# Performance work log

Measured on AMD Instinct MI355X. Metric: run time of the kernel, lower is better.

The kernel has to match this reference:

```python
import jax, jax.numpy as jnp
import numpy as np

B, D = 8192, 128


def setup_inputs() -> dict:
    key = jax.random.key(0)
    ks = jax.random.split(key, 7)
    s = 1.0 / np.sqrt(D)  # torch Linear default init scale
    x = jax.random.normal(ks[0], (B, D), jnp.float32)
    W1 = jax.random.uniform(ks[1], (D, D), jnp.float32, -s, s)
    b1 = jax.random.uniform(ks[2], (D,), jnp.float32, -s, s)
    Wmu = jax.random.uniform(ks[3], (D, D), jnp.float32, -s, s)
    bmu = jax.random.uniform(ks[4], (D,), jnp.float32, -s, s)
    Wls = jax.random.uniform(ks[5], (D, D), jnp.float32, -s, s)
    bls = jax.random.uniform(ks[6], (D,), jnp.float32, -s, s)
    return {"x": x, "W1": W1, "b1": b1, "Wmu": Wmu, "bmu": bmu, "Wls": Wls, "bls": bls}


def reference(x, W1, b1, Wmu, bmu, Wls, bls):
    d = x.shape[1]
    mask = jnp.tril(jnp.ones((d, d), x.dtype), -1)  # strict lower triangular, as in MaskedLinear
    W1m = W1 * mask
    Wmum = Wmu * mask
    Wlsm = Wls * mask

    def step(carry, i):
        z, ldj = carry
        h = jax.nn.relu(z @ W1m.T + b1)          # [B, D] hidden (MaskedLinear + ReLU)
        # only column i of mu/logs is consumed each step -> use weight row i
        mu_i = h @ Wmum[i] + bmu[i]              # [B]
        logs_i = h @ Wlsm[i] + bls[i]            # [B]
        z = z.at[:, i].set(mu_i + x[:, i] * jnp.exp(logs_i))
        return (z, ldj + logs_i), None

    z0 = jnp.zeros_like(x)
    ldj0 = jnp.zeros(x.shape[0], x.dtype)
    (z, ldj), _ = jax.lax.scan(step, (z0, ldj0), jnp.arange(d))
    return z, ldj
```

## Files before the change

### kernel.cpp

```cpp
#include <hip/hip_runtime.h>
#include <stdint.h>

#define D 128

typedef float f2 __attribute__((ext_vector_type(2)));
typedef float f4 __attribute__((ext_vector_type(4)));

__device__ __forceinline__ uint16_t f2bf(float f) {
  uint32_t u = __float_as_uint(f);
  u += 0x7fffu + ((u >> 16) & 1u);
  return (uint16_t)(u >> 16);
}
__device__ __forceinline__ uint32_t pkbf(float a, float b) {
  return (uint32_t)f2bf(a) | ((uint32_t)f2bf(b) << 16);
}
__device__ __forceinline__ f2 unpkbf(uint32_t u) {
  f2 r;
  r.x = __uint_as_float(u << 16);
  r.y = __uint_as_float(u & 0xffff0000u);
  return r;
}
__device__ __forceinline__ float rdlane(float v, int l) {
  return __int_as_float(__builtin_amdgcn_readlane(__float_as_int(v), l));
}

#define WS_NEED (size_t)(3 * 32 * 64 * 16)

__global__ __launch_bounds__(256)
void iaf_prep(const float* __restrict__ W1, const float* __restrict__ Wmu,
              const float* __restrict__ Wls, uint4* __restrict__ ws) {
  const int t = blockIdx.x * 256 + threadIdx.x;
  if (t >= 32 * 64) return;
  const int jb = t >> 6, l = t & 63;
  const int k0 = 2 * l, k1 = 2 * l + 1;
  uint32_t mm[4], ll[4], ww[4];
#pragma unroll
  for (int c = 0; c < 4; ++c) {
    const int j = jb * 4 + c;
    const float m0 = (j < k0) ? Wmu[k0 * D + j] : 0.f;
    const float m1 = (j < k1) ? Wmu[k1 * D + j] : 0.f;
    const float s0 = (j < k0) ? Wls[k0 * D + j] : 0.f;
    const float s1 = (j < k1) ? Wls[k1 * D + j] : 0.f;
    const float w0 = (j < k0) ? W1[k0 * D + j] : 0.f;
    const float w1_ = (j < k1) ? W1[k1 * D + j] : 0.f;
    mm[c] = pkbf(m0, m1);
    ll[c] = pkbf(s0, s1);
    ww[c] = pkbf(w0, w1_);
  }
  uint4 m4, l4, w4;
  m4.x = mm[0]; m4.y = mm[1]; m4.z = mm[2]; m4.w = mm[3];
  l4.x = ll[0]; l4.y = ll[1]; l4.z = ll[2]; l4.w = ll[3];
  w4.x = ww[0]; w4.y = ww[1]; w4.z = ww[2]; w4.w = ww[3];
  ws[t] = m4;
  ws[2048 + t] = l4;
  ws[4096 + t] = w4;
}

#define SEL(U, c) ((c) == 0 ? (U).x : (c) == 1 ? (U).y : (c) == 2 ? (U).z : (U).w)
#define E(V, c) (((c) & 1) ? (V).y : (V).x)

#define STEP(c, M4, L4, W4, JB)                                           \
  {                                                                       \
    const int Ln = (JB) * 2 + ((c) >> 1);                                 \
    const f2 wm = unpkbf(SEL(M4, c));                                     \
    const f2 wl = unpkbf(SEL(L4, c));                                     \
    const f2 wv = unpkbf(SEL(W4, c));                                     \
    const float hA = fmaxf(E(paA, c), 0.f);                               \
    const float hB = fmaxf(E(paB, c), 0.f);                               \
    const float zA =                                                      \
        fmaf(E(xA, c), __expf(E(plsA, c) + E(blsR, c)), E(pmuA, c) + E(bmuR, c)); \
    const float zB =                                                      \
        fmaf(E(xB, c), __expf(E(plsB, c) + E(blsR, c)), E(pmuB, c) + E(bmuR, c)); \
    const float szA = rdlane(zA, Ln);                                     \
    const float shA = rdlane(hA, Ln);                                     \
    const float szB = rdlane(zB, Ln);                                     \
    const float shB = rdlane(hB, Ln);                                     \
    f2 t;                                                                 \
    t.x = szA; t.y = szA;                                                 \
    paA = __builtin_elementwise_fma(t, wv, paA);                          \
    t.x = shA; t.y = shA;                                                 \
    pmuA = __builtin_elementwise_fma(t, wm, pmuA);                        \
    plsA = __builtin_elementwise_fma(t, wl, plsA);                        \
    t.x = szB; t.y = szB;                                                 \
    paB = __builtin_elementwise_fma(t, wv, paB);                          \
    t.x = shB; t.y = shB;                                                 \
    pmuB = __builtin_elementwise_fma(t, wm, pmuB);                        \
    plsB = __builtin_elementwise_fma(t, wl, plsB);                        \
  }

__global__ __launch_bounds__(1024, 1)
void iaf_main(const float* __restrict__ x, const float* __restrict__ b1,
              const float* __restrict__ bmu, const float* __restrict__ bls,
              const uint4* __restrict__ ws, float* __restrict__ out, int B) {
  __shared__ uint4 wsh[3 * 2048];

  const int tid = threadIdx.x;
#pragma unroll
  for (int k = 0; k < 6; ++k) wsh[tid + k * 1024] = ws[tid + k * 1024];

  const int lane = tid & 63;
  const int wave = tid >> 6;
  const int rA = blockIdx.x * 32 + wave * 2;
  const int rB = rA + 1;
  const int l2 = lane * 2;

  const f2 xA = *(const f2*)(x + (size_t)rA * D + l2);
  const f2 xB = *(const f2*)(x + (size_t)rB * D + l2);
  const f2 b1R = *(const f2*)(b1 + l2);
  const f2 bmuR = *(const f2*)(bmu + l2);
  const f2 blsR = *(const f2*)(bls + l2);

  f2 paA = b1R, paB = b1R;
  f2 pmuA = (f2)0.f, pmuB = (f2)0.f;
  f2 plsA = (f2)0.f, plsB = (f2)0.f;

  const uint4* wmu4s = wsh;
  const uint4* wls4s = wsh + 2048;
  const uint4* w14s = wsh + 4096;

  __syncthreads();

  uint4 mC = wmu4s[lane], lC = wls4s[lane], wC = w14s[lane];

#pragma unroll 1
  for (int jb = 0; jb < 32; ++jb) {
    const int nb = (jb + 1 < 32) ? jb + 1 : 31;
    const uint4 mN = wmu4s[nb * 64 + lane];
    const uint4 lN = wls4s[nb * 64 + lane];
    const uint4 wN = w14s[nb * 64 + lane];
    STEP(0, mC, lC, wC, jb)
    STEP(1, mC, lC, wC, jb)
    STEP(2, mC, lC, wC, jb)
    STEP(3, mC, lC, wC, jb)
    mC = mN; lC = lN; wC = wN;
  }

  f2 zfA, zfB;
  zfA.x = fmaf(xA.x, __expf(plsA.x + blsR.x), pmuA.x + bmuR.x);
  zfA.y = fmaf(xA.y, __expf(plsA.y + blsR.y), pmuA.y + bmuR.y);
  zfB.x = fmaf(xB.x, __expf(plsB.x + blsR.x), pmuB.x + bmuR.x);
  zfB.y = fmaf(xB.y, __expf(plsB.y + blsR.y), pmuB.y + bmuR.y);
  *(f2*)(out + (size_t)rA * D + l2) = zfA;
  *(f2*)(out + (size_t)rB * D + l2) = zfB;

  float ldjA = (plsA.x + blsR.x) + (plsA.y + blsR.y);
  float ldjB = (plsB.x + blsR.x) + (plsB.y + blsR.y);
#pragma unroll
  for (int m = 1; m < 64; m <<= 1) {
    ldjA += __shfl_xor(ldjA, m);
    ldjB += __shfl_xor(ldjB, m);
  }
  if (lane == 0) {
    out[(size_t)B * D + rA] = ldjA;
    out[(size_t)B * D + rB] = ldjB;
  }
}

#define FNTHR 256
#define FRPB 16
#define W1S 136
template <int CTRL>
__device__ __forceinline__ float dppmov(float v) {
  return __int_as_float(
      __builtin_amdgcn_update_dpp(0, __float_as_int(v), CTRL, 0xf, 0xf, true));
}
#define DPP_ADD(v, ctrl) (v) += dppmov<(ctrl)>((v))
__device__ __forceinline__ f2 unpk(uint32_t u) {
  f2 r;
  r.x = __uint_as_float(u << 16);
  r.y = __uint_as_float(u & 0xffff0000u);
  return r;
}
#define RED16F(v)      \
  do {                 \
    DPP_ADD(v, 0xB1);  \
    DPP_ADD(v, 0x4E);  \
    DPP_ADD(v, 0x124); \
    DPP_ADD(v, 0x128); \
  } while (0)
#define FSTEP(I, XE, ZRE, MKE, WM0, WM1, WL0, WL1)                  \
  {                                                                 \
    const float bmu_i = bmu[(I)];                                   \
    const float bls_i = bls[(I)];                                   \
    const f2 h0 = __builtin_elementwise_max(A0, (f2)0.f);           \
    const f2 h1 = __builtin_elementwise_max(A1, (f2)0.f);           \
    const f2 h2_ = __builtin_elementwise_max(A2, (f2)0.f);          \
    const f2 h3 = __builtin_elementwise_max(A3, (f2)0.f);           \
    const f2 q0 = h0 * mk0, q1 = h1 * mk1;                          \
    const f2 q2 = h2_ * mk2, q3 = h3 * mk3;                         \
    f2 am = q0 * WM0.xy;                                            \
    f2 al = q0 * WL0.xy;                                            \
    am = __builtin_elementwise_fma(q1, WM0.zw, am);                 \
    al = __builtin_elementwise_fma(q1, WL0.zw, al);                 \
    am = __builtin_elementwise_fma(q2, WM1.xy, am);                 \
    al = __builtin_elementwise_fma(q2, WL1.xy, al);                 \
    am = __builtin_elementwise_fma(q3, WM1.zw, am);                 \
    al = __builtin_elementwise_fma(q3, WL1.zw, al);                 \
    float mu_p = am.x + am.y;                                       \
    float ls_p = al.x + al.y;                                       \
    {                                                               \
      const int pfr = ((I) + 2 < D) ? (I) + 2 : D - 1;              \
      WM0 = *(const f4*)(wmup + pfr * D);                           \
      WM1 = *(const f4*)(wmup + pfr * D + 4);                       \
      WL0 = *(const f4*)(wlsp + pfr * D);                           \
      WL1 = *(const f4*)(wlsp + pfr * D + 4);                       \
    }                                                               \
    RED16F(mu_p);                                                   \
    RED16F(ls_p);                                                   \
    const float mu_t = mu_p + bmu_i;                                \
    const float ls_t = ls_p + bls_i;                                \
    const float zi = fmaf((XE), __expf(ls_t), mu_t);                \
    ldj += ls_t;                                                    \
    const uint4 wv = *(const uint4*)(w1p + (I)*W1S);                \
    if (own) {                                                      \
      ZRE = zi;                                                     \
      MKE = 1.f;                                                    \
    }                                                               \
    f2 zz;                                                          \
    zz.x = zi;                                                      \
    zz.y = zi;                                                      \
    A0 = __builtin_elementwise_fma(zz, unpk(wv.x), A0);             \
    A1 = __builtin_elementwise_fma(zz, unpk(wv.y), A1);             \
    A2 = __builtin_elementwise_fma(zz, unpk(wv.z), A2);             \
    A3 = __builtin_elementwise_fma(zz, unpk(wv.w), A3);             \
  }

__global__ __launch_bounds__(FNTHR, 2)
void iaf_fb(const float* __restrict__ x, const float* __restrict__ W1,
            const float* __restrict__ b1, const float* __restrict__ Wmu,
            const float* __restrict__ bmu, const float* __restrict__ Wls,
            const float* __restrict__ bls, float* __restrict__ out, int B) {
  __shared__ uint16_t w1c[D * W1S];
  const int tid = threadIdx.x;
  for (int idx = tid; idx < D * D; idx += FNTHR) {
    const int p = idx >> 7, q = idx & (D - 1);
    w1c[q * W1S + p] = f2bf((p > q) ? W1[idx] : 0.f);
  }
  __syncthreads();
  const int lane = tid & 63;
  const int m = lane & 15;
  const int row = blockIdx.x * FRPB + (tid >> 4);
  const float* __restrict__ xp = x + (size_t)row * D;
  const float* __restrict__ wmup = Wmu + m * 8;
  const float* __restrict__ wlsp = Wls + m * 8;
  const uint16_t* __restrict__ w1p = w1c + m * 8;
  f2 A0, A1, A2, A3;
  {
    const f4 t0 = *(const f4*)(b1 + m * 8);
    const f4 t1 = *(const f4*)(b1 + m * 8 + 4);
    A0 = t0.xy; A1 = t0.zw; A2 = t1.xy; A3 = t1.zw;
  }
  f2 mk0 = (f2)0.f, mk1 = (f2)0.f, mk2 = (f2)0.f, mk3 = (f2)0.f;
  float zr0 = 0, zr1 = 0, zr2 = 0, zr3 = 0, zr4 = 0, zr5 = 0, zr6 = 0, zr7 = 0;
  float ldj = 0.f;
  f4 wmA0 = *(const f4*)(wmup);
  f4 wmA1 = *(const f4*)(wmup + 4);
  f4 wlA0 = *(const f4*)(wlsp);
  f4 wlA1 = *(const f4*)(wlsp + 4);
  f4 wmB0 = *(const f4*)(wmup + D);
  f4 wmB1 = *(const f4*)(wmup + D + 4);
  f4 wlB0 = *(const f4*)(wlsp + D);
  f4 wlB1 = *(const f4*)(wlsp + D + 4);
  f4 x4a = *(const f4*)(xp);
  f4 x4b;
  for (int ib = 0; ib < 16; ++ib) {
    const int i0 = ib * 8;
    const bool own = (m == ib);
    x4b = *(const f4*)(xp + i0 + 4);
    FSTEP(i0 + 0, x4a.x, zr0, mk0.x, wmA0, wmA1, wlA0, wlA1);
    FSTEP(i0 + 1, x4a.y, zr1, mk0.y, wmB0, wmB1, wlB0, wlB1);
    FSTEP(i0 + 2, x4a.z, zr2, mk1.x, wmA0, wmA1, wlA0, wlA1);
    FSTEP(i0 + 3, x4a.w, zr3, mk1.y, wmB0, wmB1, wlB0, wlB1);
    {
      const int nx = (i0 + 8 < D) ? i0 + 8 : D - 4;
      x4a = *(const f4*)(xp + nx);
    }
    FSTEP(i0 + 4, x4b.x, zr4, mk2.x, wmA0, wmA1, wlA0, wlA1);
    FSTEP(i0 + 5, x4b.y, zr5, mk2.y, wmB0, wmB1, wlB0, wlB1);
    FSTEP(i0 + 6, x4b.z, zr6, mk3.x, wmA0, wmA1, wlA0, wlA1);
    FSTEP(i0 + 7, x4b.w, zr7, mk3.y, wmB0, wmB1, wlB0, wlB1);
  }
  f4 o0, o1;
  o0.x = zr0; o0.y = zr1; o0.z = zr2; o0.w = zr3;
  o1.x = zr4; o1.y = zr5; o1.z = zr6; o1.w = zr7;
  float* zo = out + (size_t)row * D + m * 8;
  *(f4*)(zo) = o0;
  *(f4*)(zo + 4) = o1;
  if (m == 0) out[(size_t)B * D + row] = ldj;
}

extern "C" void kernel_launch(void* const* d_in, const int* in_sizes, int n_in,
                              void* d_out, int out_size, void* d_ws, size_t ws_size,
                              hipStream_t stream) {
  const float* x   = (const float*)d_in[0];
  const float* W1  = (const float*)d_in[1];
  const float* b1  = (const float*)d_in[2];
  const float* Wmu = (const float*)d_in[3];
  const float* bmu = (const float*)d_in[4];
  const float* Wls = (const float*)d_in[5];
  const float* bls = (const float*)d_in[6];
  float* out = (float*)d_out;

  const int B = in_sizes[0] / D;

  if (ws_size >= WS_NEED) {
    iaf_prep<<<8, 256, 0, stream>>>(W1, Wmu, Wls, (uint4*)d_ws);
    const int grid = (B + 31) / 32;
    iaf_main<<<grid, 1024, 0, stream>>>(x, b1, bmu, bls, (const uint4*)d_ws, out, B);
  } else {
    const int grid = (B + FRPB - 1) / FRPB;
    iaf_fb<<<grid, FNTHR, 0, stream>>>(x, W1, b1, Wmu, bmu, Wls, bls, out, B);
  }
}
```

Before: 44.54 us.

## Use one row per wave, stream W1 from global, fold biases and log2e

Each wave now processes one batch row instead of two, so the grid doubles and the launch bound asks for more resident waves per CU. W1 weights are read from global memory (cache) rather than LDS, cutting LDS use so more blocks fit. Biases are folded into the accumulator initial values and log2(e) is pre-multiplied into Wls so exp becomes a raw exp2, with the log-determinant rescaled by ln2 at the end. The trade-off is less instruction-level parallelism per wave, since the two interleaved independent chains are gone, in exchange for higher occupancy, plus extra global-load latency inside the serial loop.

```diff
diff --git a/kernel.cpp b/kernel.cpp
--- a/kernel.cpp
+++ b/kernel.cpp
@@ -2,6 +2,8 @@
 #include <stdint.h>
 
 #define D 128
+#define LOG2E 1.4426950408889634f
+#define LN2 0.6931471805599453f
 
 typedef float f2 __attribute__((ext_vector_type(2)));
 typedef float f4 __attribute__((ext_vector_type(4)));
@@ -23,8 +25,15 @@
 __device__ __forceinline__ float rdlane(float v, int l) {
   return __int_as_float(__builtin_amdgcn_readlane(__float_as_int(v), l));
 }
-
-#define WS_NEED (size_t)(3 * 32 * 64 * 16)
+__device__ __forceinline__ float exp2x(float v) {
+#if __has_builtin(__builtin_amdgcn_exp2f)
+  return __builtin_amdgcn_exp2f(v);
+#else
+  return exp2f(v);
+#endif
+}
+
+#define WS_NEED (size_t)(3 * 2048 * 16)
 
 __global__ __launch_bounds__(256)
 void iaf_prep(const float* __restrict__ W1, const float* __restrict__ Wmu,
@@ -39,8 +48,8 @@
     const int j = jb * 4 + c;
     const float m0 = (j < k0) ? Wmu[k0 * D + j] : 0.f;
     const float m1 = (j < k1) ? Wmu[k1 * D + j] : 0.f;
-    const float s0 = (j < k0) ? Wls[k0 * D + j] : 0.f;
-    const float s1 = (j < k1) ? Wls[k1 * D + j] : 0.f;
+    const float s0 = (j < k0) ? Wls[k0 * D + j] * LOG2E : 0.f;
+    const float s1 = (j < k1) ? Wls[k1 * D + j] * LOG2E : 0.f;
     const float w0 = (j < k0) ? W1[k0 * D + j] : 0.f;
     const float w1_ = (j < k1) ? W1[k1 * D + j] : 0.f;
     mm[c] = pkbf(m0, m1);
@@ -59,101 +68,80 @@
 #define SEL(U, c) ((c) == 0 ? (U).x : (c) == 1 ? (U).y : (c) == 2 ? (U).z : (U).w)
 #define E(V, c) (((c) & 1) ? (V).y : (V).x)
 
-#define STEP(c, M4, L4, W4, JB)                                           \
-  {                                                                       \
-    const int Ln = (JB) * 2 + ((c) >> 1);                                 \
-    const f2 wm = unpkbf(SEL(M4, c));                                     \
-    const f2 wl = unpkbf(SEL(L4, c));                                     \
-    const f2 wv = unpkbf(SEL(W4, c));                                     \
-    const float hA = fmaxf(E(paA, c), 0.f);                               \
-    const float hB = fmaxf(E(paB, c), 0.f);                               \
-    const float zA =                                                      \
-        fmaf(E(xA, c), __expf(E(plsA, c) + E(blsR, c)), E(pmuA, c) + E(bmuR, c)); \
-    const float zB =                                                      \
-        fmaf(E(xB, c), __expf(E(plsB, c) + E(blsR, c)), E(pmuB, c) + E(bmuR, c)); \
-    const float szA = rdlane(zA, Ln);                                     \
-    const float shA = rdlane(hA, Ln);                                     \
-    const float szB = rdlane(zB, Ln);                                     \
-    const float shB = rdlane(hB, Ln);                                     \
-    f2 t;                                                                 \
-    t.x = szA; t.y = szA;                                                 \
-    paA = __builtin_elementwise_fma(t, wv, paA);                          \
-    t.x = shA; t.y = shA;                                                 \
-    pmuA = __builtin_elementwise_fma(t, wm, pmuA);                        \
-    plsA = __builtin_elementwise_fma(t, wl, plsA);                        \
-    t.x = szB; t.y = szB;                                                 \
-    paB = __builtin_elementwise_fma(t, wv, paB);                          \
-    t.x = shB; t.y = shB;                                                 \
-    pmuB = __builtin_elementwise_fma(t, wm, pmuB);                        \
-    plsB = __builtin_elementwise_fma(t, wl, plsB);                        \
-  }
-
-__global__ __launch_bounds__(1024, 1)
+#define STEP(c)                                                   \
+  {                                                               \
+    const int Ln = jb * 2 + ((c) >> 1);                           \
+    const f2 wm = unpkbf(SEL(mC, c));                             \
+    const f2 wl = unpkbf(SEL(lC, c));                             \
+    const f2 wv = unpkbf(SEL(wC, c));                             \
+    const float h = fmaxf(E(pa, c), 0.f);                         \
+    const float z = fmaf(E(xR, c), exp2x(E(pls, c)), E(pmu, c));  \
+    const float sz = rdlane(z, Ln);                               \
+    const float sh = rdlane(h, Ln);                               \
+    f2 t;                                                         \
+    t.x = sz; t.y = sz;                                           \
+    pa = __builtin_elementwise_fma(t, wv, pa);                    \
+    t.x = sh; t.y = sh;                                           \
+    pmu = __builtin_elementwise_fma(t, wm, pmu);                  \
+    pls = __builtin_elementwise_fma(t, wl, pls);                  \
+  }
+
+__global__ __launch_bounds__(1024, 8)
 void iaf_main(const float* __restrict__ x, const float* __restrict__ b1,
               const float* __restrict__ bmu, const float* __restrict__ bls,
               const uint4* __restrict__ ws, float* __restrict__ out, int B) {
-  __shared__ uint4 wsh[3 * 2048];
+  __shared__ uint4 wsh[2 * 2048];
 
   const int tid = threadIdx.x;
 #pragma unroll
-  for (int k = 0; k < 6; ++k) wsh[tid + k * 1024] = ws[tid + k * 1024];
+  for (int k = 0; k < 4; ++k) wsh[tid + k * 1024] = ws[tid + k * 1024];
 
   const int lane = tid & 63;
   const int wave = tid >> 6;
-  const int rA = blockIdx.x * 32 + wave * 2;
-  const int rB = rA + 1;
+  const int row = blockIdx.x * 16 + wave;
   const int l2 = lane * 2;
 
-  const f2 xA = *(const f2*)(x + (size_t)rA * D + l2);
-  const f2 xB = *(const f2*)(x + (size_t)rB * D + l2);
-  const f2 b1R = *(const f2*)(b1 + l2);
-  const f2 bmuR = *(const f2*)(bmu + l2);
-  const f2 blsR = *(const f2*)(bls + l2);
-
-  f2 paA = b1R, paB = b1R;
-  f2 pmuA = (f2)0.f, pmuB = (f2)0.f;
-  f2 plsA = (f2)0.f, plsB = (f2)0.f;
+  const f2 xR = *(const f2*)(x + (size_t)row * D + l2);
+  f2 pa = *(const f2*)(b1 + l2);
+  f2 pmu = *(const f2*)(bmu + l2);
+  f2 pls = *(const f2*)(bls + l2);
+  pls.x *= LOG2E;
+  pls.y *= LOG2E;
 
   const uint4* wmu4s = wsh;
   const uint4* wls4s = wsh + 2048;
-  const uint4* w14s = wsh + 4096;
+  const uint4* w14g = ws + 4096;
 
   __syncthreads();
 
-  uint4 mC = wmu4s[lane], lC = wls4s[lane], wC = w14s[lane];
+  uint4 mC = wmu4s[lane];
+  uint4 lC = wls4s[lane];
+  uint4 wC = w14g[lane];
 
 #pragma unroll 1
   for (int jb = 0; jb < 32; ++jb) {
     const int nb = (jb + 1 < 32) ? jb + 1 : 31;
     const uint4 mN = wmu4s[nb * 64 + lane];
     const uint4 lN = wls4s[nb * 64 + lane];
-    const uint4 wN = w14s[nb * 64 + lane];
-    STEP(0, mC, lC, wC, jb)
-    STEP(1, mC, lC, wC, jb)
-    STEP(2, mC, lC, wC, jb)
-    STEP(3, mC, lC, wC, jb)
-    mC = mN; lC = lN; wC = wN;
-  }
-
-  f2 zfA, zfB;
-  zfA.x = fmaf(xA.x, __expf(plsA.x + blsR.x), pmuA.x + bmuR.x);
-  zfA.y = fmaf(xA.y, __expf(plsA.y + blsR.y), pmuA.y + bmuR.y);
-  zfB.x = fmaf(xB.x, __expf(plsB.x + blsR.x), pmuB.x + bmuR.x);
-  zfB.y = fmaf(xB.y, __expf(plsB.y + blsR.y), pmuB.y + bmuR.y);
-  *(f2*)(out + (size_t)rA * D + l2) = zfA;
-  *(f2*)(out + (size_t)rB * D + l2) = zfB;
-
-  float ldjA = (plsA.x + blsR.x) + (plsA.y + blsR.y);
-  float ldjB = (plsB.x + blsR.x) + (plsB.y + blsR.y);
+    const uint4 wN = w14g[nb * 64 + lane];
+    STEP(0)
+    STEP(1)
+    STEP(2)
+    STEP(3)
+    mC = mN;
+    lC = lN;
+    wC = wN;
+  }
+
+  f2 zf;
+  zf.x = fmaf(xR.x, exp2x(pls.x), pmu.x);
+  zf.y = fmaf(xR.y, exp2x(pls.y), pmu.y);
+  *(f2*)(out + (size_t)row * D + l2) = zf;
+
+  float ldj = pls.x + pls.y;
 #pragma unroll
-  for (int m = 1; m < 64; m <<= 1) {
-    ldjA += __shfl_xor(ldjA, m);
-    ldjB += __shfl_xor(ldjB, m);
-  }
-  if (lane == 0) {
-    out[(size_t)B * D + rA] = ldjA;
-    out[(size_t)B * D + rB] = ldjB;
-  }
+  for (int m2 = 1; m2 < 64; m2 <<= 1) ldj += __shfl_xor(ldj, m2);
+  if (lane == 0) out[(size_t)B * D + row] = ldj * LN2;
 }
 
 #define FNTHR 256
@@ -305,7 +293,7 @@
 
   if (ws_size >= WS_NEED) {
     iaf_prep<<<8, 256, 0, stream>>>(W1, Wmu, Wls, (uint4*)d_ws);
-    const int grid = (B + 31) / 32;
+    const int grid = (B + 15) / 16;
     iaf_main<<<grid, 1024, 0, stream>>>(x, b1, bmu, bls, (const uint4*)d_ws, out, B);
   } else {
     const int grid = (B + FRPB - 1) / FRPB;
```

Measured after the change: 44.55 us. Within noise of the previous version (+0.0%).
